# Kernel tuning notes

Hardware: AMD Instinct MI355X
Metric: run time of the kernel (lower is better)

Reference implementation:

```python
import jax, jax.numpy as jnp
import numpy as np

TAU = 100.0
DT = 1.0
NOISE_STD = 0.1
HID = 100


def setup_inputs() -> dict:
    key = jax.random.key(0)
    ks = jax.random.split(key, 7)
    T, B = 750, 1024
    input_seq = jax.random.normal(ks[0], (T, B, 4), dtype=jnp.float32)
    noise = jax.random.normal(ks[1], (T, B, HID), dtype=jnp.float32)
    # orthogonal recurrent weight J [H, H]
    a = jax.random.normal(ks[2], (HID, HID), dtype=jnp.float32)
    q, r = jnp.linalg.qr(a)
    J_w = q * jnp.sign(jnp.diag(r))[None, :]
    # input projection rows [b_m; b_c; b_cm; b_cc] -> [4, H] (xavier for (H,1) fan)
    bound_b = float(np.sqrt(6.0 / (HID + 1)))
    Bmat = jax.random.uniform(ks[3], (4, HID), jnp.float32, -bound_b, bound_b)
    c_x = jnp.zeros((HID,), dtype=jnp.float32)
    bound_w = float(np.sqrt(6.0 / (HID + 1)))
    Wout_w = jax.random.uniform(ks[4], (1, HID), jnp.float32, -bound_w, bound_w)
    Wout_b = jnp.zeros((1,), dtype=jnp.float32)
    return {"input_seq": input_seq, "noise": noise, "J_w": J_w,
            "Bmat": Bmat, "c_x": c_x, "Wout_w": Wout_w, "Wout_b": Wout_b}


def reference(input_seq, noise, J_w, Bmat, c_x, Wout_w, Wout_b):
    # input_seq: [T, B, 4], noise: [T, B, H]
    T, B, _ = input_seq.shape
    alpha = DT / TAU

    # precompute input drive for all steps: u_m@b_m^T + ... == u_t @ Bmat  [T, B, H]
    drive = jnp.einsum('tbi,ih->tbh', input_seq, Bmat)

    def step(x, inp):
        d_t, n_t = inp
        r = jnp.tanh(x)
        dx = alpha * (-x + r @ J_w.T + d_t + c_x + NOISE_STD * n_t)
        x = x + dx
        return x, None

    x0 = jnp.zeros((B, HID), dtype=input_seq.dtype)
    x_final, _ = jax.lax.scan(step, x0, (drive, noise))
    out = jnp.tanh(x_final) @ Wout_w.T + Wout_b  # [B, 1]
    return out.squeeze(-1)  # [B]
```

## Files before the change

kernel.cpp:

```cpp
#include <hip/hip_runtime.h>
#include <hip/hip_bf16.h>

#define HID 100
#define TT 750
#define NB_TOT 1024
#define ALPHA 0.01f
#define NSTD 0.1f

typedef __bf16 bf16x8 __attribute__((ext_vector_type(8)));
typedef float floatx4 __attribute__((ext_vector_type(4)));

__device__ __forceinline__ float fast_tanh(float v) {
    float e = __expf(2.0f * v);
    return 1.0f - 2.0f / (e + 1.0f);
}

__global__ __launch_bounds__(256, 2)
void rnn_kernel(const float* __restrict__ useq,
                const float* __restrict__ noise,
                const float* __restrict__ Jw,
                const float* __restrict__ Bm,
                const float* __restrict__ cxp,
                const float* __restrict__ Ww,
                const float* __restrict__ Wb,
                float* __restrict__ out)
{
    __shared__ __align__(16) __bf16 rbuf[16 * 128];
    __shared__ float ybuf[2][112];
    __shared__ float red[256];

    const int tid  = threadIdx.x;
    const int wv   = tid >> 6;
    const int lane = tid & 63;
    const int wg   = blockIdx.x;

    const int  bb  = tid / 100;
    const int  hh  = tid % 100;
    const bool upd = (tid < 200);
    const int  gb  = wg * 2 + bb;

    float bm0=0.f, bm1=0.f, bm2=0.f, bm3=0.f, cx=0.f, wout=0.f;
    if (upd) {
        bm0 = Bm[0*HID + hh]; bm1 = Bm[1*HID + hh];
        bm2 = Bm[2*HID + hh]; bm3 = Bm[3*HID + hh];
        cx  = cxp[hh];
        wout = Ww[hh];
    }

    {
        floatx4 z = {0.f, 0.f, 0.f, 0.f};
        ((floatx4*)rbuf)[tid] = z;
    }

    const int m16 = lane & 15;
    const int q   = lane >> 4;
    bf16x8 jhi[2][4], jlo[2][4];
    #pragma unroll
    for (int ti = 0; ti < 2; ++ti) {
        const int tile = wv * 2 + ti;
        const int h = tile * 16 + m16;
        #pragma unroll
        for (int s = 0; s < 4; ++s) {
            bf16x8 vhi, vlo;
            #pragma unroll
            for (int j = 0; j < 8; ++j) {
                const int k = s * 32 + q * 8 + j;
                float v = (h < HID && k < HID) ? Jw[h * HID + k] : 0.0f;
                __bf16 hi = (__bf16)v;
                vhi[j] = hi;
                vlo[j] = (__bf16)(v - (float)hi);
            }
            jhi[ti][s] = vhi;
            jlo[ti][s] = vlo;
        }
    }

    const float* np = noise + (size_t)gb * HID + hh;
    const float* up = useq  + (size_t)gb * 4;
    float   nb0=0.f, nb1=0.f, nb2=0.f, nb3=0.f;
    floatx4 ub0={0,0,0,0}, ub1={0,0,0,0}, ub2={0,0,0,0}, ub3={0,0,0,0};
    if (upd) {
        nb0 = np[0 * (NB_TOT*HID)]; ub0 = *(const floatx4*)(up + 0 * (NB_TOT*4));
        nb1 = np[1 * (NB_TOT*HID)]; ub1 = *(const floatx4*)(up + 1 * (NB_TOT*4));
        nb2 = np[2 * (NB_TOT*HID)]; ub2 = *(const floatx4*)(up + 2 * (NB_TOT*4));
        nb3 = np[3 * (NB_TOT*HID)]; ub3 = *(const floatx4*)(up + 3 * (NB_TOT*4));
    }

    float x = 0.0f;
    __syncthreads();

    auto step = [&](int T, float& NB, floatx4& UB) {
        bf16x8 afr[4];
        const bf16x8* rb16 = (const bf16x8*)rbuf;
        #pragma unroll
        for (int s = 0; s < 4; ++s)
            afr[s] = rb16[m16 * 16 + ((s * 4 + q) ^ (lane & 7))];
        #pragma unroll
        for (int ti = 0; ti < 2; ++ti) {
            floatx4 acc = {0.f, 0.f, 0.f, 0.f};
            #pragma unroll
            for (int s = 0; s < 4; ++s)
                acc = __builtin_amdgcn_mfma_f32_16x16x32_bf16(afr[s], jhi[ti][s], acc, 0, 0, 0);
            #pragma unroll
            for (int s = 0; s < 4; ++s)
                acc = __builtin_amdgcn_mfma_f32_16x16x32_bf16(afr[s], jlo[ti][s], acc, 0, 0, 0);
            const int tile = wv * 2 + ti;
            if (tile < 7 && lane < 16) {
                ybuf[0][tile * 16 + lane] = acc[0];
                ybuf[1][tile * 16 + lane] = acc[1];
            }
        }
        __syncthreads();
        if (upd) {
            const float y = ybuf[bb][hh];
            const float d = UB[0]*bm0 + UB[1]*bm1 + UB[2]*bm2 + UB[3]*bm3;
            x = x * (1.0f - ALPHA) + ALPHA * (y + d + cx + NSTD * NB);
            const float r = fast_tanh(x);
            rbuf[bb * 128 + (((hh >> 3) ^ bb) << 3) + (hh & 7)] = (__bf16)r;
            const int tf = (T + 4 < TT) ? (T + 4) : (TT - 1);
            NB = np[tf * (NB_TOT*HID)];
            UB = *(const floatx4*)(up + tf * (NB_TOT*4));
        }
        __syncthreads();
    };

    for (int tb = 0; tb < 748; tb += 4) {
        step(tb + 0, nb0, ub0);
        step(tb + 1, nb1, ub1);
        step(tb + 2, nb2, ub2);
        step(tb + 3, nb3, ub3);
    }
    step(748, nb0, ub0);
    step(749, nb1, ub1);

    red[tid] = upd ? (fast_tanh(x) * wout) : 0.0f;
    __syncthreads();
    if (tid < 2) {
        float s2 = Wb[0];
        #pragma unroll 4
        for (int i = 0; i < HID; ++i) s2 += red[tid * HID + i];
        out[wg * 2 + tid] = s2;
    }
}

extern "C" void kernel_launch(void* const* d_in, const int* in_sizes, int n_in,
                              void* d_out, int out_size, void* d_ws, size_t ws_size,
                              hipStream_t stream) {
    rnn_kernel<<<dim3(512), dim3(256), 0, stream>>>(
        (const float*)d_in[0], (const float*)d_in[1], (const float*)d_in[2],
        (const float*)d_in[3], (const float*)d_in[4], (const float*)d_in[5],
        (const float*)d_in[6], (float*)d_out);
}
```

Before: 723.5 us.

## Update state from MFMA accumulators directly with double-buffered r, four batches per block

The hidden-state update now runs in the lanes that hold the MFMA outputs, so the ybuf round-trip through shared memory and one barrier per step go away. The r buffer is double-buffered so each step needs only a single __syncthreads. Each block now processes four batch rows instead of two, with half as many blocks and the launch bounds relaxed to one block per SM. The hi and lo products accumulate separately and are summed afterwards. Fewer lanes do the elementwise work (only q==0 lanes), which serializes 4 batches per lane and halves grid parallelism.

```diff
diff --git a/kernel.cpp b/kernel.cpp
--- a/kernel.cpp
+++ b/kernel.cpp
@@ -3,7 +3,7 @@
 
 #define HID 100
 #define TT 750
-#define NB_TOT 1024
+#define NBT 1024
 #define ALPHA 0.01f
 #define NSTD 0.1f
 
@@ -15,7 +15,7 @@
     return 1.0f - 2.0f / (e + 1.0f);
 }
 
-__global__ __launch_bounds__(256, 2)
+__global__ __launch_bounds__(256, 1)
 void rnn_kernel(const float* __restrict__ useq,
                 const float* __restrict__ noise,
                 const float* __restrict__ Jw,
@@ -25,35 +25,25 @@
                 const float* __restrict__ Wb,
                 float* __restrict__ out)
 {
-    __shared__ __align__(16) __bf16 rbuf[16 * 128];
-    __shared__ float ybuf[2][112];
-    __shared__ float red[256];
+    __shared__ __align__(16) __bf16 rbuf[2][16 * 128];
+    __shared__ float red[4][8][16];
 
     const int tid  = threadIdx.x;
     const int wv   = tid >> 6;
     const int lane = tid & 63;
+    const int m16  = lane & 15;
+    const int q    = lane >> 4;
     const int wg   = blockIdx.x;
-
-    const int  bb  = tid / 100;
-    const int  hh  = tid % 100;
-    const bool upd = (tid < 200);
-    const int  gb  = wg * 2 + bb;
-
-    float bm0=0.f, bm1=0.f, bm2=0.f, bm3=0.f, cx=0.f, wout=0.f;
-    if (upd) {
-        bm0 = Bm[0*HID + hh]; bm1 = Bm[1*HID + hh];
-        bm2 = Bm[2*HID + hh]; bm3 = Bm[3*HID + hh];
-        cx  = cxp[hh];
-        wout = Ww[hh];
-    }
+    const int gb0  = wg * 4;
 
     {
         floatx4 z = {0.f, 0.f, 0.f, 0.f};
-        ((floatx4*)rbuf)[tid] = z;
+        ((floatx4*)rbuf)[tid]       = z;
+        ((floatx4*)rbuf)[tid + 256] = z;
+        ((float*)red)[tid]       = 0.f;
+        ((float*)red)[tid + 256] = 0.f;
     }
 
-    const int m16 = lane & 15;
-    const int q   = lane >> 4;
     bf16x8 jhi[2][4], jlo[2][4];
     #pragma unroll
     for (int ti = 0; ti < 2; ++ti) {
@@ -75,78 +65,112 @@
         }
     }
 
-    const float* np = noise + (size_t)gb * HID + hh;
-    const float* up = useq  + (size_t)gb * 4;
-    float   nb0=0.f, nb1=0.f, nb2=0.f, nb3=0.f;
-    floatx4 ub0={0,0,0,0}, ub1={0,0,0,0}, ub2={0,0,0,0}, ub3={0,0,0,0};
-    if (upd) {
-        nb0 = np[0 * (NB_TOT*HID)]; ub0 = *(const floatx4*)(up + 0 * (NB_TOT*4));
-        nb1 = np[1 * (NB_TOT*HID)]; ub1 = *(const floatx4*)(up + 1 * (NB_TOT*4));
-        nb2 = np[2 * (NB_TOT*HID)]; ub2 = *(const floatx4*)(up + 2 * (NB_TOT*4));
-        nb3 = np[3 * (NB_TOT*HID)]; ub3 = *(const floatx4*)(up + 3 * (NB_TOT*4));
+    int   hv[2];
+    bool  val[2];
+    float bmv[2][4], cxv[2], wwv[2];
+    #pragma unroll
+    for (int ti = 0; ti < 2; ++ti) {
+        const int tile = wv * 2 + ti;
+        const int h = tile * 16 + m16;
+        hv[ti]  = h;
+        val[ti] = (q == 0) && (h < HID);
+        if (val[ti]) {
+            bmv[ti][0] = Bm[0*HID + h]; bmv[ti][1] = Bm[1*HID + h];
+            bmv[ti][2] = Bm[2*HID + h]; bmv[ti][3] = Bm[3*HID + h];
+            cxv[ti] = cxp[h];
+            wwv[ti] = Ww[h];
+        } else {
+            bmv[ti][0]=bmv[ti][1]=bmv[ti][2]=bmv[ti][3]=0.f; cxv[ti]=0.f; wwv[ti]=0.f;
+        }
     }
 
-    float x = 0.0f;
+    float   nA[2][4], nB[2][4];
+    floatx4 uA[4], uB[4];
+    auto pfN = [&](int t, float (&N)[2][4]) {
+        #pragma unroll
+        for (int ti = 0; ti < 2; ++ti) {
+            if (val[ti]) {
+                const float* p = noise + (size_t)t * (NBT * HID) + (size_t)gb0 * HID + hv[ti];
+                #pragma unroll
+                for (int b = 0; b < 4; ++b) N[ti][b] = p[b * HID];
+            }
+        }
+    };
+    auto pfU = [&](int t, floatx4 (&U)[4]) {
+        const floatx4* p = (const floatx4*)(useq + (size_t)t * (NBT * 4) + (size_t)gb0 * 4);
+        #pragma unroll
+        for (int b = 0; b < 4; ++b) U[b] = p[b];
+    };
+    pfN(0, nA); pfU(0, uA);
+    pfN(1, nB); pfU(1, uB);
+
+    float x[2][4] = {{0.f,0.f,0.f,0.f},{0.f,0.f,0.f,0.f}};
     __syncthreads();
 
-    auto step = [&](int T, float& NB, floatx4& UB) {
+    auto step = [&](int t, int pb, float (&N)[2][4], floatx4 (&U)[4]) {
+        const bf16x8* rb = (const bf16x8*)(rbuf[pb]);
         bf16x8 afr[4];
-        const bf16x8* rb16 = (const bf16x8*)rbuf;
         #pragma unroll
         for (int s = 0; s < 4; ++s)
-            afr[s] = rb16[m16 * 16 + ((s * 4 + q) ^ (lane & 7))];
+            afr[s] = rb[m16 * 16 + ((s * 4 + q) ^ (lane & 7))];
+        floatx4 ys[2];
         #pragma unroll
         for (int ti = 0; ti < 2; ++ti) {
-            floatx4 acc = {0.f, 0.f, 0.f, 0.f};
+            floatx4 ah = {0.f,0.f,0.f,0.f}, al = {0.f,0.f,0.f,0.f};
             #pragma unroll
             for (int s = 0; s < 4; ++s)
-                acc = __builtin_amdgcn_mfma_f32_16x16x32_bf16(afr[s], jhi[ti][s], acc, 0, 0, 0);
+                ah = __builtin_amdgcn_mfma_f32_16x16x32_bf16(afr[s], jhi[ti][s], ah, 0, 0, 0);
             #pragma unroll
             for (int s = 0; s < 4; ++s)
-                acc = __builtin_amdgcn_mfma_f32_16x16x32_bf16(afr[s], jlo[ti][s], acc, 0, 0, 0);
-            const int tile = wv * 2 + ti;
-            if (tile < 7 && lane < 16) {
-                ybuf[0][tile * 16 + lane] = acc[0];
-                ybuf[1][tile * 16 + lane] = acc[1];
+                al = __builtin_amdgcn_mfma_f32_16x16x32_bf16(afr[s], jlo[ti][s], al, 0, 0, 0);
+            ys[ti] = ah + al;
+        }
+        __bf16* wbuf = rbuf[pb ^ 1];
+        #pragma unroll
+        for (int ti = 0; ti < 2; ++ti) {
+            if (val[ti]) {
+                #pragma unroll
+                for (int b = 0; b < 4; ++b) {
+                    const float d = U[b][0]*bmv[ti][0] + U[b][1]*bmv[ti][1]
+                                  + U[b][2]*bmv[ti][2] + U[b][3]*bmv[ti][3];
+                    x[ti][b] = x[ti][b] * (1.0f - ALPHA)
+                             + ALPHA * (ys[ti][b] + d + cxv[ti] + NSTD * N[ti][b]);
+                    const float r = fast_tanh(x[ti][b]);
+                    wbuf[b * 128 + (((hv[ti] >> 3) ^ b) << 3) + (hv[ti] & 7)] = (__bf16)r;
+                }
             }
         }
-        __syncthreads();
-        if (upd) {
-            const float y = ybuf[bb][hh];
-            const float d = UB[0]*bm0 + UB[1]*bm1 + UB[2]*bm2 + UB[3]*bm3;
-            x = x * (1.0f - ALPHA) + ALPHA * (y + d + cx + NSTD * NB);
-            const float r = fast_tanh(x);
-            rbuf[bb * 128 + (((hh >> 3) ^ bb) << 3) + (hh & 7)] = (__bf16)r;
-            const int tf = (T + 4 < TT) ? (T + 4) : (TT - 1);
-            NB = np[tf * (NB_TOT*HID)];
-            UB = *(const floatx4*)(up + tf * (NB_TOT*4));
-        }
+        int tf = t + 2; if (tf > TT - 1) tf = TT - 1;
+        pfN(tf, N); pfU(tf, U);
         __syncthreads();
     };
 
-    for (int tb = 0; tb < 748; tb += 4) {
-        step(tb + 0, nb0, ub0);
-        step(tb + 1, nb1, ub1);
-        step(tb + 2, nb2, ub2);
-        step(tb + 3, nb3, ub3);
+    for (int t2 = 0; t2 < TT; t2 += 2) {
+        step(t2,     0, nA, uA);
+        step(t2 + 1, 1, nB, uB);
     }
-    step(748, nb0, ub0);
-    step(749, nb1, ub1);
 
-    red[tid] = upd ? (fast_tanh(x) * wout) : 0.0f;
+    #pragma unroll
+    for (int ti = 0; ti < 2; ++ti) {
+        if (val[ti]) {
+            #pragma unroll
+            for (int b = 0; b < 4; ++b)
+                red[b][wv * 2 + ti][m16] = fast_tanh(x[ti][b]) * wwv[ti];
+        }
+    }
     __syncthreads();
-    if (tid < 2) {
-        float s2 = Wb[0];
-        #pragma unroll 4
-        for (int i = 0; i < HID; ++i) s2 += red[tid * HID + i];
-        out[wg * 2 + tid] = s2;
+    if (tid < 4) {
+        float s = Wb[0];
+        #pragma unroll 8
+        for (int j = 0; j < 112; ++j) s += red[tid][j >> 4][j & 15];
+        out[gb0 + tid] = s;
     }
 }
 
 extern "C" void kernel_launch(void* const* d_in, const int* in_sizes, int n_in,
                               void* d_out, int out_size, void* d_ws, size_t ws_size,
                               hipStream_t stream) {
-    rnn_kernel<<<dim3(512), dim3(256), 0, stream>>>(
+    rnn_kernel<<<dim3(256), dim3(256), 0, stream>>>(
         (const float*)d_in[0], (const float*)d_in[1], (const float*)d_in[2],
         (const float*)d_in[3], (const float*)d_in[4], (const float*)d_in[5],
         (const float*)d_in[6], (float*)d_out);
```

New measurement: 1.219 ms. 1.69x slower.

## Fold input drive and bias into MFMA, one barrier per step with 4 batches per block

Applied to the files above, without the earlier changes.

Restructures the recurrence so each block handles 4 batch rows with 7 waves, one 16-row output tile per wave. The input projection and bias are packed into the K padding of the bf16 hi/lo matmul, with the input split into hi/lo parts and a constant 1 column. The y result is kept in registers and the shared ybuf handoff is removed. A double-buffered activation buffer reduces the step to a single s_waitcnt plus barrier instead of two __syncthreads. In exchange, the grid halves to 256 blocks, most MFMA A-rows are zero (only every fourth row is used), and a hand-written barrier asm is added.

```diff
diff --git a/kernel.cpp b/kernel.cpp
--- a/kernel.cpp
+++ b/kernel.cpp
@@ -3,11 +3,12 @@
 
 #define HID 100
 #define TT 750
-#define NB_TOT 1024
+#define NBT 1024
 #define ALPHA 0.01f
 #define NSTD 0.1f
 
 typedef __bf16 bf16x8 __attribute__((ext_vector_type(8)));
+typedef __bf16 bf16x4 __attribute__((ext_vector_type(4)));
 typedef float floatx4 __attribute__((ext_vector_type(4)));
 
 __device__ __forceinline__ float fast_tanh(float v) {
@@ -15,7 +16,7 @@
     return 1.0f - 2.0f / (e + 1.0f);
 }
 
-__global__ __launch_bounds__(256, 2)
+__global__ __launch_bounds__(448, 2)
 void rnn_kernel(const float* __restrict__ useq,
                 const float* __restrict__ noise,
                 const float* __restrict__ Jw,
@@ -25,128 +26,142 @@
                 const float* __restrict__ Wb,
                 float* __restrict__ out)
 {
-    __shared__ __align__(16) __bf16 rbuf[16 * 128];
-    __shared__ float ybuf[2][112];
-    __shared__ float red[256];
+    __shared__ __align__(16) __bf16 abuf[2][4 * 128];
+    __shared__ float red[4][112];
 
     const int tid  = threadIdx.x;
     const int wv   = tid >> 6;
     const int lane = tid & 63;
-    const int wg   = blockIdx.x;
+    const int m16  = lane & 15;
+    const int q    = lane >> 4;
+    const int h    = wv * 16 + m16;
+    const bool act = (h < HID);
+    const int gb0  = blockIdx.x * 4;
 
-    const int  bb  = tid / 100;
-    const int  hh  = tid % 100;
-    const bool upd = (tid < 200);
-    const int  gb  = wg * 2 + bb;
+    if (tid < 128) ((floatx4*)abuf)[tid] = floatx4{0.f, 0.f, 0.f, 0.f};
 
-    float bm0=0.f, bm1=0.f, bm2=0.f, bm3=0.f, cx=0.f, wout=0.f;
-    if (upd) {
-        bm0 = Bm[0*HID + hh]; bm1 = Bm[1*HID + hh];
-        bm2 = Bm[2*HID + hh]; bm3 = Bm[3*HID + hh];
-        cx  = cxp[hh];
-        wout = Ww[hh];
+    bf16x8 jhi[4], jlo[4];
+    #pragma unroll
+    for (int s = 0; s < 4; ++s) {
+        bf16x8 vh = {}; bf16x8 vl = {};
+        #pragma unroll
+        for (int j = 0; j < 8; ++j) {
+            const int k = s * 32 + q * 8 + j;
+            float a = 0.f; bool lo = false;
+            if (act) {
+                if (k < HID)        { a = Jw[h * HID + k];        lo = true; }
+                else if (k < 104)   { a = Bm[(k - 100) * HID + h]; lo = true; }
+                else if (k < 108)   { a = Bm[(k - 104) * HID + h]; lo = false; }
+                else if (k == 108)  { a = cxp[h];                  lo = true; }
+            }
+            const __bf16 hi = (__bf16)a;
+            vh[j] = hi;
+            vl[j] = lo ? (__bf16)(a - (float)hi) : (__bf16)0.f;
+        }
+        jhi[s] = vh; jlo[s] = vl;
     }
 
-    {
-        floatx4 z = {0.f, 0.f, 0.f, 0.f};
-        ((floatx4*)rbuf)[tid] = z;
+    __syncthreads();
+
+    if (tid < 4) {
+        const floatx4 u0 = *(const floatx4*)(useq + (size_t)(gb0 + tid) * 4);
+        bf16x4 uh, ul;
+        #pragma unroll
+        for (int i = 0; i < 4; ++i) {
+            const __bf16 hi = (__bf16)u0[i];
+            uh[i] = hi; ul[i] = (__bf16)(u0[i] - (float)hi);
+        }
+        *(bf16x4*)&abuf[0][tid * 128 + ((12 ^ (tid << 2)) << 3) + 4] = uh;
+        *(bf16x4*)&abuf[0][tid * 128 + ((13 ^ (tid << 2)) << 3)]     = ul;
+        abuf[0][tid * 128 + ((13 ^ (tid << 2)) << 3) + 4] = (__bf16)1.0f;
+        abuf[1][tid * 128 + ((13 ^ (tid << 2)) << 3) + 4] = (__bf16)1.0f;
     }
 
-    const int m16 = lane & 15;
-    const int q   = lane >> 4;
-    bf16x8 jhi[2][4], jlo[2][4];
-    #pragma unroll
-    for (int ti = 0; ti < 2; ++ti) {
-        const int tile = wv * 2 + ti;
-        const int h = tile * 16 + m16;
+    const float* nptr = noise + (size_t)(gb0 + q) * HID + h;
+    float n0 = 0.f, n1 = 0.f, n2 = 0.f, n3 = 0.f;
+    if (act) {
+        n0 = nptr[(size_t)0 * NBT * HID];
+        n1 = nptr[(size_t)1 * NBT * HID];
+        n2 = nptr[(size_t)2 * NBT * HID];
+        n3 = nptr[(size_t)3 * NBT * HID];
+    }
+    floatx4 us0 = {}, us1 = {}, us2 = {}, us3 = {};
+    if (tid < 4) {
+        us1 = *(const floatx4*)(useq + (size_t)1 * NBT * 4 + (gb0 + tid) * 4);
+        us2 = *(const floatx4*)(useq + (size_t)2 * NBT * 4 + (gb0 + tid) * 4);
+        us3 = *(const floatx4*)(useq + (size_t)3 * NBT * 4 + (gb0 + tid) * 4);
+        us0 = *(const floatx4*)(useq + (size_t)4 * NBT * 4 + (gb0 + tid) * 4);
+    }
+
+    float x = 0.f;
+    __syncthreads();
+
+    auto body = [&](int t, int p, float& nr, floatx4& ur) {
+        const int br = m16 >> 2;
+        bf16x8 afr[4];
         #pragma unroll
         for (int s = 0; s < 4; ++s) {
-            bf16x8 vhi, vlo;
-            #pragma unroll
-            for (int j = 0; j < 8; ++j) {
-                const int k = s * 32 + q * 8 + j;
-                float v = (h < HID && k < HID) ? Jw[h * HID + k] : 0.0f;
-                __bf16 hi = (__bf16)v;
-                vhi[j] = hi;
-                vlo[j] = (__bf16)(v - (float)hi);
-            }
-            jhi[ti][s] = vhi;
-            jlo[ti][s] = vlo;
+            bf16x8 a = {};
+            if ((m16 & 3) == 0)
+                a = *(const bf16x8*)&abuf[p][br * 128 + ((((s << 2) | q) ^ (br << 2)) << 3)];
+            afr[s] = a;
         }
-    }
-
-    const float* np = noise + (size_t)gb * HID + hh;
-    const float* up = useq  + (size_t)gb * 4;
-    float   nb0=0.f, nb1=0.f, nb2=0.f, nb3=0.f;
-    floatx4 ub0={0,0,0,0}, ub1={0,0,0,0}, ub2={0,0,0,0}, ub3={0,0,0,0};
-    if (upd) {
-        nb0 = np[0 * (NB_TOT*HID)]; ub0 = *(const floatx4*)(up + 0 * (NB_TOT*4));
-        nb1 = np[1 * (NB_TOT*HID)]; ub1 = *(const floatx4*)(up + 1 * (NB_TOT*4));
-        nb2 = np[2 * (NB_TOT*HID)]; ub2 = *(const floatx4*)(up + 2 * (NB_TOT*4));
-        nb3 = np[3 * (NB_TOT*HID)]; ub3 = *(const floatx4*)(up + 3 * (NB_TOT*4));
-    }
-
-    float x = 0.0f;
-    __syncthreads();
-
-    auto step = [&](int T, float& NB, floatx4& UB) {
-        bf16x8 afr[4];
-        const bf16x8* rb16 = (const bf16x8*)rbuf;
+        floatx4 ah = {0.f,0.f,0.f,0.f}, al = {0.f,0.f,0.f,0.f};
         #pragma unroll
         for (int s = 0; s < 4; ++s)
-            afr[s] = rb16[m16 * 16 + ((s * 4 + q) ^ (lane & 7))];
+            ah = __builtin_amdgcn_mfma_f32_16x16x32_bf16(afr[s], jhi[s], ah, 0, 0, 0);
         #pragma unroll
-        for (int ti = 0; ti < 2; ++ti) {
-            floatx4 acc = {0.f, 0.f, 0.f, 0.f};
+        for (int s = 0; s < 4; ++s)
+            al = __builtin_amdgcn_mfma_f32_16x16x32_bf16(afr[s], jlo[s], al, 0, 0, 0);
+        const float y = ah[0] + al[0];
+
+        if (tid < 4) {
+            bf16x4 uh, ul;
             #pragma unroll
-            for (int s = 0; s < 4; ++s)
-                acc = __builtin_amdgcn_mfma_f32_16x16x32_bf16(afr[s], jhi[ti][s], acc, 0, 0, 0);
-            #pragma unroll
-            for (int s = 0; s < 4; ++s)
-                acc = __builtin_amdgcn_mfma_f32_16x16x32_bf16(afr[s], jlo[ti][s], acc, 0, 0, 0);
-            const int tile = wv * 2 + ti;
-            if (tile < 7 && lane < 16) {
-                ybuf[0][tile * 16 + lane] = acc[0];
-                ybuf[1][tile * 16 + lane] = acc[1];
+            for (int i = 0; i < 4; ++i) {
+                const __bf16 hi = (__bf16)ur[i];
+                uh[i] = hi; ul[i] = (__bf16)(ur[i] - (float)hi);
             }
+            *(bf16x4*)&abuf[p ^ 1][tid * 128 + ((12 ^ (tid << 2)) << 3) + 4] = uh;
+            *(bf16x4*)&abuf[p ^ 1][tid * 128 + ((13 ^ (tid << 2)) << 3)]     = ul;
+            const int tu = (t + 5 <= TT - 1) ? (t + 5) : (TT - 1);
+            ur = *(const floatx4*)(useq + (size_t)tu * NBT * 4 + (gb0 + tid) * 4);
         }
-        __syncthreads();
-        if (upd) {
-            const float y = ybuf[bb][hh];
-            const float d = UB[0]*bm0 + UB[1]*bm1 + UB[2]*bm2 + UB[3]*bm3;
-            x = x * (1.0f - ALPHA) + ALPHA * (y + d + cx + NSTD * NB);
+
+        if (act) {
+            x = x * (1.f - ALPHA) + ALPHA * (y + NSTD * nr);
             const float r = fast_tanh(x);
-            rbuf[bb * 128 + (((hh >> 3) ^ bb) << 3) + (hh & 7)] = (__bf16)r;
-            const int tf = (T + 4 < TT) ? (T + 4) : (TT - 1);
-            NB = np[tf * (NB_TOT*HID)];
-            UB = *(const floatx4*)(up + tf * (NB_TOT*4));
+            abuf[p ^ 1][q * 128 + (((h >> 3) ^ (q << 2)) << 3) + (h & 7)] = (__bf16)r;
+            const int tn = (t + 4 <= TT - 1) ? (t + 4) : (TT - 1);
+            nr = nptr[(size_t)tn * NBT * HID];
         }
-        __syncthreads();
+
+        asm volatile("s_waitcnt lgkmcnt(0)\n\ts_barrier" ::: "memory");
     };
 
-    for (int tb = 0; tb < 748; tb += 4) {
-        step(tb + 0, nb0, ub0);
-        step(tb + 1, nb1, ub1);
-        step(tb + 2, nb2, ub2);
-        step(tb + 3, nb3, ub3);
+    for (int t4 = 0; t4 < 748; t4 += 4) {
+        body(t4 + 0, 0, n0, us1);
+        body(t4 + 1, 1, n1, us2);
+        body(t4 + 2, 0, n2, us3);
+        body(t4 + 3, 1, n3, us0);
     }
-    step(748, nb0, ub0);
-    step(749, nb1, ub1);
+    body(748, 0, n0, us1);
+    body(749, 1, n1, us2);
 
-    red[tid] = upd ? (fast_tanh(x) * wout) : 0.0f;
+    if (act) red[q][h] = fast_tanh(x) * Ww[h];
     __syncthreads();
-    if (tid < 2) {
-        float s2 = Wb[0];
+    if (tid < 4) {
+        float s = Wb[0];
         #pragma unroll 4
-        for (int i = 0; i < HID; ++i) s2 += red[tid * HID + i];
-        out[wg * 2 + tid] = s2;
+        for (int i = 0; i < HID; ++i) s += red[tid][i];
+        out[gb0 + tid] = s;
     }
 }
 
 extern "C" void kernel_launch(void* const* d_in, const int* in_sizes, int n_in,
                               void* d_out, int out_size, void* d_ws, size_t ws_size,
                               hipStream_t stream) {
-    rnn_kernel<<<dim3(512), dim3(256), 0, stream>>>(
+    rnn_kernel<<<dim3(256), dim3(448), 0, stream>>>(
         (const float*)d_in[0], (const float*)d_in[1], (const float*)d_in[2],
         (const float*)d_in[3], (const float*)d_in[4], (const float*)d_in[5],
         (const float*)d_in[6], (float*)d_out);
```

Measured after the change: 881.3 us. 21.8% more time.
